# Performance work log

Hardware: AMD Instinct MI355X
Metric: run time of the kernel (lower is better)

The kernel has to match this reference:

```python
import jax, jax.numpy as jnp
import numpy as np

EPS = 1e-5

def rational(x, a, b):
    # Rational activation version 'A': P(x)/(1+|Q(x)|), deg(P)=5, deg(Q)=4 (no constant term)
    P = a[0] + x * (a[1] + x * (a[2] + x * (a[3] + x * (a[4] + x * a[5]))))
    Q = 1.0 + jnp.abs(x * (b[0] + x * (b[1] + x * (b[2] + x * b[3]))))
    return P / Q

def batch_norm(x, gamma, beta):
    # training-mode BN: per-channel batch statistics over (N,H,W), biased variance
    mean = jnp.mean(x, axis=(0, 2, 3), keepdims=True)
    var = jnp.var(x, axis=(0, 2, 3), keepdims=True)
    xn = (x - mean) * jax.lax.rsqrt(var + EPS)
    return xn * gamma[None, :, None, None] + beta[None, :, None, None]

def conv3x3(x, w):
    return jax.lax.conv_general_dilated(
        x, w, window_strides=(1, 1), padding='SAME',
        dimension_numbers=('NCHW', 'OIHW', 'NCHW'))

def multi_variant_rationals(out, ar, br, ag, bg, ab, bb):
    # channels 0::3 -> r rational, 1::3 -> g, 2::3 -> b; scatter back interleaved
    B, C, H, W = out.shape
    r = rational(out[:, 0::3], ar, br)  # (B, C//3, H, W)
    g = rational(out[:, 1::3], ag, bg)
    b = rational(out[:, 2::3], ab, bb)
    return jnp.stack([r, g, b], axis=2).reshape(B, C, H, W)

# Rational init coefficients (leaky-relu-like Pade approximant, standard rational_activations init)
_A0 = np.array([0.0218, 0.5, 1.5957, 1.1915, 0.5, 0.0891], dtype=np.float32)
_B0 = np.array([2.383, 0.0, 1.0, 0.0], dtype=np.float32)

def setup_inputs() -> dict:
    key = jax.random.key(0)
    ks = jax.random.split(key, 4)
    B, C, H, W = 64, 3, 512, 512
    x = jax.random.normal(ks[0], (B, C, H, W), dtype=jnp.float32)
    fan = C * 9
    w1 = jax.random.normal(ks[1], (C, C, 3, 3), dtype=jnp.float32) / np.sqrt(fan)
    w2 = jax.random.normal(ks[2], (C, C, 3, 3), dtype=jnp.float32) / np.sqrt(fan)
    g1 = jnp.ones((C,), jnp.float32); b1 = jnp.zeros((C,), jnp.float32)
    g2 = jnp.ones((C,), jnp.float32); b2 = jnp.zeros((C,), jnp.float32)
    ar = jnp.asarray(_A0); br = jnp.asarray(_B0)
    ag = jnp.asarray(_A0); bg = jnp.asarray(_B0)
    ab = jnp.asarray(_A0); bb = jnp.asarray(_B0)
    return {"x": x, "w1": w1, "g1": g1, "b1": b1, "ar": ar, "br": br,
            "ag": ag, "bg": bg, "ab": ab, "bb": bb, "w2": w2, "g2": g2, "b2": b2}

def reference(x, w1, g1, b1, ar, br, ag, bg, ab, bb, w2, g2, b2):
    out = conv3x3(x, w1)
    out = batch_norm(out, g1, b1)
    out = multi_variant_rationals(out, ar, br, ag, bg, ab, bb)
    out = conv3x3(out, w2)
    out = batch_norm(out, g2, b2)
    out = out + x  # identity shortcut (downsample=False)
    out = multi_variant_rationals(out, ar, br, ag, bg, ab, bb)
    return out
```

## Files before the change

### kernel.cpp

```cpp
#include <hip/hip_runtime.h>
#include <math.h>

#define HH 512
#define WW 512
#define NBATCH 64
#define PLANE (HH * WW)

#define TH2 16
#define NSTRIP (HH / TH2)
#define NWAVE (NBATCH * NSTRIP * 2)
#define NBLK2 (NWAVE / 4)
#define NPART NBLK2

#define TW 64
#define TH 16
#define NTILES (NBATCH * 8 * 32)
#define NTHR 256
#define XT_H (TH + 4)
#define XT_W (TW + 4)
#define ZT_H (TH + 2)
#define ZT_W (TW + 2)
#define X1_H (TH + 2)
#define X1_W (TW + 2)

#define Y1_ELEMS ((size_t)NBATCH * 3 * HH * WW)
#define WS_FAST_BYTES ((Y1_ELEMS + (size_t)NTILES * 6 + 16) * 4)

__device__ __forceinline__ float ratf(float v, const float* A, const float* B) {
  float p = fmaf(v, A[5], A[4]);
  p = fmaf(v, p, A[3]);
  p = fmaf(v, p, A[2]);
  p = fmaf(v, p, A[1]);
  p = fmaf(v, p, A[0]);
  float q = fmaf(v, B[3], B[2]);
  q = fmaf(v, q, B[1]);
  q = fmaf(v, q, B[0]);
  q *= v;
  float den = 1.0f + fabsf(q);
  return p * __builtin_amdgcn_rcpf(den);
}

__device__ __forceinline__ void block_reduce6_store(float s[6], float* __restrict__ dst) {
  __shared__ float red[4][6];
#pragma unroll
  for (int k = 0; k < 6; ++k) {
    float v = s[k];
#pragma unroll
    for (int off = 32; off; off >>= 1) v += __shfl_down(v, off, 64);
    s[k] = v;
  }
  int lane = threadIdx.x & 63, wv = threadIdx.x >> 6;
  if (lane == 0) {
#pragma unroll
    for (int k = 0; k < 6; ++k) red[wv][k] = s[k];
  }
  __syncthreads();
  if (threadIdx.x < 6) {
    dst[threadIdx.x] = red[0][threadIdx.x] + red[1][threadIdx.x] + red[2][threadIdx.x] + red[3][threadIdx.x];
  }
}

__global__ __launch_bounds__(256) void k_reduce(const float* __restrict__ partials, int n,
                                                const float* __restrict__ gamma,
                                                const float* __restrict__ beta,
                                                float* __restrict__ out6) {
  double s[6] = {0, 0, 0, 0, 0, 0};
  for (int j = threadIdx.x; j < n; j += 256) {
    const float* p = partials + (size_t)j * 6;
#pragma unroll
    for (int k = 0; k < 6; ++k) s[k] += (double)p[k];
  }
  __shared__ double red[256];
  __shared__ double tot[6];
  for (int k = 0; k < 6; ++k) {
    red[threadIdx.x] = s[k];
    __syncthreads();
    for (int off = 128; off; off >>= 1) {
      if (threadIdx.x < off) red[threadIdx.x] += red[threadIdx.x + off];
      __syncthreads();
    }
    if (threadIdx.x == 0) tot[k] = red[0];
    __syncthreads();
  }
  if (threadIdx.x < 3) {
    int c = threadIdx.x;
    double N = 16777216.0;
    double mean = tot[c] / N;
    double var = tot[3 + c] / N - mean * mean;
    double sc = (double)gamma[c] / sqrt(var + 1e-5);
    double sh = (double)beta[c] - mean * sc;
    out6[c] = (float)sc;
    out6[3 + c] = (float)sh;
  }
}


struct LRow {
  float4 v;
  float e;
  bool ok;
};
struct FRow {
  float4 v;
  float L, R;
};

__device__ __forceinline__ LRow load_row(const float* __restrict__ base, int gh, int c0,
                                         int lane, int elane, int eoff) {
  LRow r;
  r.v = make_float4(0.f, 0.f, 0.f, 0.f);
  r.e = 0.f;
  r.ok = ((unsigned)gh < (unsigned)HH);
  if (r.ok) {
    const float* p = base + (size_t)gh * WW + c0;
    r.v = *(const float4*)p;
    if (lane == elane) r.e = p[eoff];
  }
  return r;
}

__device__ __forceinline__ FRow fin1(const LRow& n, int lane, bool leftSeg) {
  FRow f;
  f.v = n.v;
  float Lp = __shfl_up(n.v.w, 1);
  float Rp = __shfl_down(n.v.x, 1);
  f.L = (lane == 0) ? (leftSeg ? 0.f : n.e) : Lp;
  f.R = (lane == 63) ? (leftSeg ? n.e : 0.f) : Rp;
  return f;
}

__device__ __forceinline__ FRow fin2(const LRow& n, int lane, bool leftSeg,
                                     float sc, float sh, const float* A, const float* B) {
  FRow f;
  if (!n.ok) {
    f.v = make_float4(0.f, 0.f, 0.f, 0.f);
    f.L = 0.f;
    f.R = 0.f;
    return f;
  }
  float4 z;
  z.x = ratf(fmaf(n.v.x, sc, sh), A, B);
  z.y = ratf(fmaf(n.v.y, sc, sh), A, B);
  z.z = ratf(fmaf(n.v.z, sc, sh), A, B);
  z.w = ratf(fmaf(n.v.w, sc, sh), A, B);
  float et = ratf(fmaf(n.e, sc, sh), A, B);
  float Lp = __shfl_up(z.w, 1);
  float Rp = __shfl_down(z.x, 1);
  f.v = z;
  f.L = (lane == 0) ? (leftSeg ? 0.f : et) : Lp;
  f.R = (lane == 63) ? (leftSeg ? et : 0.f) : Rp;
  return f;
}

__device__ __forceinline__ void conv_accum(const FRow (&F)[3][3], const float (&wr)[3][3][3][3],
                                           float4 (&acc)[3]) {
#pragma unroll
  for (int ci = 0; ci < 3; ++ci)
#pragma unroll
    for (int ky = 0; ky < 3; ++ky) {
      float s0 = F[ci][ky].L;
      float s1 = F[ci][ky].v.x;
      float s2 = F[ci][ky].v.y;
      float s3 = F[ci][ky].v.z;
      float s4 = F[ci][ky].v.w;
      float s5 = F[ci][ky].R;
#pragma unroll
      for (int co = 0; co < 3; ++co) {
        float w0 = wr[co][ci][ky][0], w1_ = wr[co][ci][ky][1], w2_ = wr[co][ci][ky][2];
        acc[co].x = fmaf(w0, s0, acc[co].x);
        acc[co].x = fmaf(w1_, s1, acc[co].x);
        acc[co].x = fmaf(w2_, s2, acc[co].x);
        acc[co].y = fmaf(w0, s1, acc[co].y);
        acc[co].y = fmaf(w1_, s2, acc[co].y);
        acc[co].y = fmaf(w2_, s3, acc[co].y);
        acc[co].z = fmaf(w0, s2, acc[co].z);
        acc[co].z = fmaf(w1_, s3, acc[co].z);
        acc[co].z = fmaf(w2_, s4, acc[co].z);
        acc[co].w = fmaf(w0, s3, acc[co].w);
        acc[co].w = fmaf(w1_, s4, acc[co].w);
        acc[co].w = fmaf(w2_, s5, acc[co].w);
      }
    }
}

__global__ __launch_bounds__(256) void k_conv1_v2(const float* __restrict__ x,
                                                  const float* __restrict__ w1,
                                                  float* __restrict__ y1,
                                                  float* __restrict__ partials) {
  int lane = threadIdx.x & 63;
  int wid = (blockIdx.x << 2) | (threadIdx.x >> 6);
  int seg = wid & 1;
  int strip = (wid >> 1) & (NSTRIP - 1);
  int b = wid >> 6;
  bool leftSeg = (seg == 0);
  int elane = leftSeg ? 63 : 0;
  int eoff = leftSeg ? 4 : -1;
  int c0 = (seg << 8) | (lane << 2);
  int h0 = strip * TH2;

  float wr[3][3][3][3];
#pragma unroll
  for (int o = 0; o < 3; ++o)
#pragma unroll
    for (int ci = 0; ci < 3; ++ci)
#pragma unroll
      for (int ky = 0; ky < 3; ++ky)
#pragma unroll
        for (int kx = 0; kx < 3; ++kx)
          wr[o][ci][ky][kx] = w1[((o * 3 + ci) * 3 + ky) * 3 + kx];

  const float* xb[3];
#pragma unroll
  for (int ci = 0; ci < 3; ++ci) xb[ci] = x + (size_t)(b * 3 + ci) * PLANE;
  float* yb = y1 + (size_t)(b * 3) * PLANE;

  FRow F[3][3];
  LRow N[3];
  {
    LRow P[3], Q[3];
#pragma unroll
    for (int ci = 0; ci < 3; ++ci) P[ci] = load_row(xb[ci], h0 - 1, c0, lane, elane, eoff);
#pragma unroll
    for (int ci = 0; ci < 3; ++ci) Q[ci] = load_row(xb[ci], h0, c0, lane, elane, eoff);
#pragma unroll
    for (int ci = 0; ci < 3; ++ci) N[ci] = load_row(xb[ci], h0 + 1, c0, lane, elane, eoff);
#pragma unroll
    for (int ci = 0; ci < 3; ++ci) {
      F[ci][0] = fin1(P[ci], lane, leftSeg);
      F[ci][1] = fin1(Q[ci], lane, leftSeg);
    }
  }

  float st[6] = {0.f, 0.f, 0.f, 0.f, 0.f, 0.f};
#pragma unroll 4
  for (int r = 0; r < TH2; ++r) {
#pragma unroll
    for (int ci = 0; ci < 3; ++ci) F[ci][2] = fin1(N[ci], lane, leftSeg);
    if (r < TH2 - 1) {
#pragma unroll
      for (int ci = 0; ci < 3; ++ci) N[ci] = load_row(xb[ci], h0 + r + 2, c0, lane, elane, eoff);
    }
    float4 acc[3];
    acc[0] = make_float4(0.f, 0.f, 0.f, 0.f);
    acc[1] = make_float4(0.f, 0.f, 0.f, 0.f);
    acc[2] = make_float4(0.f, 0.f, 0.f, 0.f);
    conv_accum(F, wr, acc);

    int gh = h0 + r;
    float* yrow = yb + (size_t)gh * WW + c0;
#pragma unroll
    for (int co = 0; co < 3; ++co) {
      *(float4*)(yrow + (size_t)co * PLANE) = acc[co];
      st[co] += (acc[co].x + acc[co].y) + (acc[co].z + acc[co].w);
      st[3 + co] += fmaf(acc[co].x, acc[co].x, acc[co].y * acc[co].y) +
                    fmaf(acc[co].z, acc[co].z, acc[co].w * acc[co].w);
    }
#pragma unroll
    for (int ci = 0; ci < 3; ++ci) {
      F[ci][0] = F[ci][1];
      F[ci][1] = F[ci][2];
    }
  }
  block_reduce6_store(st, partials + (size_t)blockIdx.x * 6);
}

__global__ __launch_bounds__(256) void k_conv2s_v2(const float* __restrict__ y1,
                                                   const float* __restrict__ w2,
                                                   const float* __restrict__ hdr,
                                                   const float* __restrict__ ar, const float* __restrict__ br,
                                                   const float* __restrict__ ag, const float* __restrict__ bg,
                                                   const float* __restrict__ ab_, const float* __restrict__ bb,
                                                   float* __restrict__ u,
                                                   float* __restrict__ partials) {
  int lane = threadIdx.x & 63;
  int wid = (blockIdx.x << 2) | (threadIdx.x >> 6);
  int seg = wid & 1;
  int strip = (wid >> 1) & (NSTRIP - 1);
  int b = wid >> 6;
  bool leftSeg = (seg == 0);
  int elane = leftSeg ? 63 : 0;
  int eoff = leftSeg ? 4 : -1;
  int c0 = (seg << 8) | (lane << 2);
  int h0 = strip * TH2;

  float sc1[3], sh1[3];
#pragma unroll
  for (int c = 0; c < 3; ++c) {
    sc1[c] = hdr[c];
    sh1[c] = hdr[3 + c];
  }
  float A[3][6], Bq[3][4];
#pragma unroll
  for (int i = 0; i < 6; ++i) { A[0][i] = ar[i]; A[1][i] = ag[i]; A[2][i] = ab_[i]; }
#pragma unroll
  for (int i = 0; i < 4; ++i) { Bq[0][i] = br[i]; Bq[1][i] = bg[i]; Bq[2][i] = bb[i]; }

  float wr[3][3][3][3];
#pragma unroll
  for (int o = 0; o < 3; ++o)
#pragma unroll
    for (int ci = 0; ci < 3; ++ci)
#pragma unroll
      for (int ky = 0; ky < 3; ++ky)
#pragma unroll
        for (int kx = 0; kx < 3; ++kx)
          wr[o][ci][ky][kx] = w2[((o * 3 + ci) * 3 + ky) * 3 + kx];

  const float* yb[3];
#pragma unroll
  for (int ci = 0; ci < 3; ++ci) yb[ci] = y1 + (size_t)(b * 3 + ci) * PLANE;
  float* ub = u + (size_t)(b * 3) * PLANE;

  FRow F[3][3];
  LRow N[3];
  {
    LRow P[3], Q[3];
#pragma unroll
    for (int ci = 0; ci < 3; ++ci) P[ci] = load_row(yb[ci], h0 - 1, c0, lane, elane, eoff);
#pragma unroll
    for (int ci = 0; ci < 3; ++ci) Q[ci] = load_row(yb[ci], h0, c0, lane, elane, eoff);
#pragma unroll
    for (int ci = 0; ci < 3; ++ci) N[ci] = load_row(yb[ci], h0 + 1, c0, lane, elane, eoff);
#pragma unroll
    for (int ci = 0; ci < 3; ++ci) {
      F[ci][0] = fin2(P[ci], lane, leftSeg, sc1[ci], sh1[ci], A[ci], Bq[ci]);
      F[ci][1] = fin2(Q[ci], lane, leftSeg, sc1[ci], sh1[ci], A[ci], Bq[ci]);
    }
  }

  float st[6] = {0.f, 0.f, 0.f, 0.f, 0.f, 0.f};
#pragma unroll 4
  for (int r = 0; r < TH2; ++r) {
#pragma unroll
    for (int ci = 0; ci < 3; ++ci)
      F[ci][2] = fin2(N[ci], lane, leftSeg, sc1[ci], sh1[ci], A[ci], Bq[ci]);
    if (r < TH2 - 1) {
#pragma unroll
      for (int ci = 0; ci < 3; ++ci) N[ci] = load_row(yb[ci], h0 + r + 2, c0, lane, elane, eoff);
    }
    float4 acc[3];
    acc[0] = make_float4(0.f, 0.f, 0.f, 0.f);
    acc[1] = make_float4(0.f, 0.f, 0.f, 0.f);
    acc[2] = make_float4(0.f, 0.f, 0.f, 0.f);
    conv_accum(F, wr, acc);

    int gh = h0 + r;
    float* urow = ub + (size_t)gh * WW + c0;
#pragma unroll
    for (int co = 0; co < 3; ++co) {
      *(float4*)(urow + (size_t)co * PLANE) = acc[co];
      st[co] += (acc[co].x + acc[co].y) + (acc[co].z + acc[co].w);
      st[3 + co] += fmaf(acc[co].x, acc[co].x, acc[co].y * acc[co].y) +
                    fmaf(acc[co].z, acc[co].z, acc[co].w * acc[co].w);
    }
#pragma unroll
    for (int ci = 0; ci < 3; ++ci) {
      F[ci][0] = F[ci][1];
      F[ci][1] = F[ci][2];
    }
  }
  block_reduce6_store(st, partials + (size_t)blockIdx.x * 6);
}

__global__ __launch_bounds__(256) void k_pointwise2(float* __restrict__ u,
                                                    const float* __restrict__ x,
                                                    const float* __restrict__ hdr,
                                                    const float* __restrict__ ar, const float* __restrict__ br,
                                                    const float* __restrict__ ag, const float* __restrict__ bg,
                                                    const float* __restrict__ ab_, const float* __restrict__ bb) {
  int plane = blockIdx.y;
  int c = plane % 3;
  const float* Ap = (c == 0) ? ar : ((c == 1) ? ag : ab_);
  const float* Bp = (c == 0) ? br : ((c == 1) ? bg : bb);
  float A[6], Bc[4];
#pragma unroll
  for (int i = 0; i < 6; ++i) A[i] = Ap[i];
#pragma unroll
  for (int i = 0; i < 4; ++i) Bc[i] = Bp[i];
  float sc2 = hdr[6 + c], sh2 = hdr[9 + c];

  size_t base = (size_t)plane * PLANE + (size_t)blockIdx.x * (256 * 8 * 4);
  const float4* xv = (const float4*)(x + base);
  float4* uv = (float4*)(u + base);
  float4 uu[8], xx[8];
#pragma unroll
  for (int k = 0; k < 8; ++k) uu[k] = uv[k * 256 + threadIdx.x];
#pragma unroll
  for (int k = 0; k < 8; ++k) xx[k] = xv[k * 256 + threadIdx.x];
#pragma unroll
  for (int k = 0; k < 8; ++k) {
    float4 o;
    o.x = ratf(fmaf(uu[k].x, sc2, sh2) + xx[k].x, A, Bc);
    o.y = ratf(fmaf(uu[k].y, sc2, sh2) + xx[k].y, A, Bc);
    o.z = ratf(fmaf(uu[k].z, sc2, sh2) + xx[k].z, A, Bc);
    o.w = ratf(fmaf(uu[k].w, sc2, sh2) + xx[k].w, A, Bc);
    uv[k * 256 + threadIdx.x] = o;
  }
}


__global__ __launch_bounds__(NTHR) void k_stats1(const float* __restrict__ x,
                                                 const float* __restrict__ w1,
                                                 float* __restrict__ partials) {
  __shared__ float xs[3][X1_H][X1_W];
  int bid = blockIdx.x;
  int tx = bid & 7, ty = (bid >> 3) & 31, b = bid >> 8;
  int h0 = ty * TH, w0 = tx * TW;

  const int NE = 3 * X1_H * X1_W;
  for (int i = threadIdx.x; i < NE; i += NTHR) {
    int c = i / (X1_H * X1_W);
    int rem = i - c * (X1_H * X1_W);
    int r = rem / X1_W, cc = rem - r * X1_W;
    int gh = h0 - 1 + r, gw = w0 - 1 + cc;
    float v = 0.f;
    if ((unsigned)gh < HH && (unsigned)gw < WW)
      v = x[(((size_t)b * 3 + c) * HH + gh) * WW + gw];
    xs[c][r][cc] = v;
  }
  float wr[3][3][3][3];
#pragma unroll
  for (int o = 0; o < 3; ++o)
#pragma unroll
    for (int ci = 0; ci < 3; ++ci)
#pragma unroll
      for (int ky = 0; ky < 3; ++ky)
#pragma unroll
        for (int kx = 0; kx < 3; ++kx)
          wr[o][ci][ky][kx] = w1[((o * 3 + ci) * 3 + ky) * 3 + kx];
  __syncthreads();

  int cc = threadIdx.x & 63;
  int rr0 = (threadIdx.x >> 6) * 4;
  float acc[4][3] = {};
#pragma unroll
  for (int ci = 0; ci < 3; ++ci)
#pragma unroll
    for (int kx = 0; kx < 3; ++kx) {
      float v[6];
#pragma unroll
      for (int i = 0; i < 6; ++i) v[i] = xs[ci][rr0 + i][cc + kx];
#pragma unroll
      for (int o = 0; o < 4; ++o)
#pragma unroll
        for (int ky = 0; ky < 3; ++ky) {
          float vv = v[o + ky];
#pragma unroll
          for (int co = 0; co < 3; ++co) acc[o][co] = fmaf(wr[co][ci][ky][kx], vv, acc[o][co]);
        }
    }
  float s[6] = {0.f, 0.f, 0.f, 0.f, 0.f, 0.f};
#pragma unroll
  for (int o = 0; o < 4; ++o)
#pragma unroll
    for (int co = 0; co < 3; ++co) {
      float y = acc[o][co];
      s[co] += y;
      s[3 + co] += y * y;
    }
  block_reduce6_store(s, partials + (size_t)bid * 6);
}

template <bool FINAL>
__global__ __launch_bounds__(NTHR) void k_fused(const float* __restrict__ x,
                                                const float* __restrict__ w1,
                                                const float* __restrict__ w2,
                                                const float* __restrict__ hdr,
                                                const float* __restrict__ ar, const float* __restrict__ br,
                                                const float* __restrict__ ag, const float* __restrict__ bg,
                                                const float* __restrict__ ab_, const float* __restrict__ bb,
                                                float* __restrict__ dst) {
  __shared__ float xs[3][XT_H][XT_W];
  __shared__ float zs[3][ZT_H][ZT_W];
  int bid = blockIdx.x;
  int tx = bid & 7, ty = (bid >> 3) & 31, b = bid >> 8;
  int h0 = ty * TH, w0 = tx * TW;

  const int NE = 3 * XT_H * XT_W;
  for (int i = threadIdx.x; i < NE; i += NTHR) {
    int c = i / (XT_H * XT_W);
    int rem = i - c * (XT_H * XT_W);
    int r = rem / XT_W, cc = rem - r * XT_W;
    int gh = h0 - 2 + r, gw = w0 - 2 + cc;
    float v = 0.f;
    if ((unsigned)gh < HH && (unsigned)gw < WW)
      v = x[(((size_t)b * 3 + c) * HH + gh) * WW + gw];
    xs[c][r][cc] = v;
  }

  float scale1[3], shift1[3];
#pragma unroll
  for (int c = 0; c < 3; ++c) {
    scale1[c] = hdr[c];
    shift1[c] = hdr[3 + c];
  }
  float A[3][6], Bq[3][4];
#pragma unroll
  for (int i = 0; i < 6; ++i) { A[0][i] = ar[i]; A[1][i] = ag[i]; A[2][i] = ab_[i]; }
#pragma unroll
  for (int i = 0; i < 4; ++i) { Bq[0][i] = br[i]; Bq[1][i] = bg[i]; Bq[2][i] = bb[i]; }

  float wr[3][3][3][3];
#pragma unroll
  for (int o = 0; o < 3; ++o)
#pragma unroll
    for (int ci = 0; ci < 3; ++ci)
#pragma unroll
      for (int ky = 0; ky < 3; ++ky)
#pragma unroll
        for (int kx = 0; kx < 3; ++kx)
          wr[o][ci][ky][kx] = w1[((o * 3 + ci) * 3 + ky) * 3 + kx];
  __syncthreads();

  for (int i = threadIdx.x; i < ZT_H * ZT_W; i += NTHR) {
    int r = i / ZT_W, cc = i - r * ZT_W;
    int gh = h0 - 1 + r, gw = w0 - 1 + cc;
    float z0 = 0.f, z1 = 0.f, z2 = 0.f;
    if ((unsigned)gh < HH && (unsigned)gw < WW) {
      float a0 = 0.f, a1 = 0.f, a2 = 0.f;
#pragma unroll
      for (int ci = 0; ci < 3; ++ci)
#pragma unroll
        for (int ky = 0; ky < 3; ++ky)
#pragma unroll
          for (int kx = 0; kx < 3; ++kx) {
            float v = xs[ci][r + ky][cc + kx];
            a0 = fmaf(wr[0][ci][ky][kx], v, a0);
            a1 = fmaf(wr[1][ci][ky][kx], v, a1);
            a2 = fmaf(wr[2][ci][ky][kx], v, a2);
          }
      z0 = ratf(fmaf(a0, scale1[0], shift1[0]), A[0], Bq[0]);
      z1 = ratf(fmaf(a1, scale1[1], shift1[1]), A[1], Bq[1]);
      z2 = ratf(fmaf(a2, scale1[2], shift1[2]), A[2], Bq[2]);
    }
    zs[0][r][cc] = z0;
    zs[1][r][cc] = z1;
    zs[2][r][cc] = z2;
  }

#pragma unroll
  for (int o = 0; o < 3; ++o)
#pragma unroll
    for (int ci = 0; ci < 3; ++ci)
#pragma unroll
      for (int ky = 0; ky < 3; ++ky)
#pragma unroll
        for (int kx = 0; kx < 3; ++kx)
          wr[o][ci][ky][kx] = w2[((o * 3 + ci) * 3 + ky) * 3 + kx];
  __syncthreads();

  int cc = threadIdx.x & 63;
  int rr0 = (threadIdx.x >> 6) * 4;
  float acc[4][3] = {};
#pragma unroll
  for (int ci = 0; ci < 3; ++ci)
#pragma unroll
    for (int kx = 0; kx < 3; ++kx) {
      float v[6];
#pragma unroll
      for (int i = 0; i < 6; ++i) v[i] = zs[ci][rr0 + i][cc + kx];
#pragma unroll
      for (int o = 0; o < 4; ++o)
#pragma unroll
        for (int ky = 0; ky < 3; ++ky) {
          float vv = v[o + ky];
#pragma unroll
          for (int co = 0; co < 3; ++co) acc[o][co] = fmaf(wr[co][ci][ky][kx], vv, acc[o][co]);
        }
    }

  if constexpr (FINAL) {
    float scale2[3], shift2[3];
#pragma unroll
    for (int c = 0; c < 3; ++c) {
      scale2[c] = hdr[6 + c];
      shift2[c] = hdr[9 + c];
    }
#pragma unroll
    for (int o = 0; o < 4; ++o) {
      int rr = rr0 + o;
#pragma unroll
      for (int co = 0; co < 3; ++co) {
        float y = fmaf(acc[o][co], scale2[co], shift2[co]);
        float v = y + xs[co][rr + 2][cc + 2];
        dst[(((size_t)b * 3 + co) * HH + (h0 + rr)) * WW + (w0 + cc)] = ratf(v, A[co], Bq[co]);
      }
    }
  } else {
    float s[6] = {0.f, 0.f, 0.f, 0.f, 0.f, 0.f};
#pragma unroll
    for (int o = 0; o < 4; ++o)
#pragma unroll
      for (int co = 0; co < 3; ++co) {
        float y = acc[o][co];
        s[co] += y;
        s[3 + co] += y * y;
      }
    block_reduce6_store(s, dst + (size_t)bid * 6);
  }
}

extern "C" void kernel_launch(void* const* d_in, const int* in_sizes, int n_in,
                              void* d_out, int out_size, void* d_ws, size_t ws_size,
                              hipStream_t stream) {
  const float* x  = (const float*)d_in[0];
  const float* w1 = (const float*)d_in[1];
  const float* g1 = (const float*)d_in[2];
  const float* b1 = (const float*)d_in[3];
  const float* ar = (const float*)d_in[4];
  const float* br = (const float*)d_in[5];
  const float* ag = (const float*)d_in[6];
  const float* bg = (const float*)d_in[7];
  const float* ab = (const float*)d_in[8];
  const float* bb = (const float*)d_in[9];
  const float* w2 = (const float*)d_in[10];
  const float* g2 = (const float*)d_in[11];
  const float* b2 = (const float*)d_in[12];
  float* out = (float*)d_out;

  if (ws_size >= WS_FAST_BYTES) {
    float* y1    = (float*)d_ws;
    float* part2 = (float*)d_ws + Y1_ELEMS;
    float* hdr   = part2 + (size_t)NPART * 6;
    float* part1 = out;

    k_conv1_v2<<<dim3(NBLK2), dim3(256), 0, stream>>>(x, w1, y1, part1);
    k_reduce<<<dim3(1), dim3(256), 0, stream>>>(part1, NPART, g1, b1, hdr);
    k_conv2s_v2<<<dim3(NBLK2), dim3(256), 0, stream>>>(y1, w2, hdr, ar, br, ag, bg, ab, bb, out, part2);
    k_reduce<<<dim3(1), dim3(256), 0, stream>>>(part2, NPART, g2, b2, hdr + 6);
    k_pointwise2<<<dim3(PLANE / (256 * 8 * 4), NBATCH * 3), dim3(256), 0, stream>>>(
        out, x, hdr, ar, br, ag, bg, ab, bb);
  } else {
    float* part1 = out;
    float* part2 = out + (size_t)NTILES * 6;
    float* hdr = (float*)d_ws;

    k_stats1<<<dim3(NTILES), dim3(NTHR), 0, stream>>>(x, w1, part1);
    k_reduce<<<dim3(1), dim3(256), 0, stream>>>(part1, NTILES, g1, b1, hdr);
    k_fused<false><<<dim3(NTILES), dim3(NTHR), 0, stream>>>(x, w1, w2, hdr, ar, br, ag, bg, ab, bb, part2);
    k_reduce<<<dim3(1), dim3(256), 0, stream>>>(part2, NTILES, g2, b2, hdr + 6);
    k_fused<true><<<dim3(NTILES), dim3(NTHR), 0, stream>>>(x, w1, w2, hdr, ar, br, ag, bg, ab, bb, out);
  }
}
```

Before: 621.5 us.

## Restructure conv row loop to scatter each input row into rotating accumulators

Both conv kernels now process each input row once, adding its contribution to three rotating output accumulators (one per kernel row) instead of keeping a three-row window of finished inputs and recomputing a full 3x3 stencil per output row. This drops the two extra FRow windows per channel in exchange for three float4 accumulator sets, with the aim of cutting register pressure and the row-shift copies. Output is emitted when an accumulator has received all three kernel rows. The main loop is hand-unrolled in groups of three with special prologue and epilogue steps, which adds some code size.

```diff
diff --git a/kernel.cpp b/kernel.cpp
--- a/kernel.cpp
+++ b/kernel.cpp
@@ -152,35 +152,75 @@
   return f;
 }
 
-__device__ __forceinline__ void conv_accum(const FRow (&F)[3][3], const float (&wr)[3][3][3][3],
-                                           float4 (&acc)[3]) {
+template <int KY>
+__device__ __forceinline__ void addrow(const FRow (&F)[3], const float (&wr)[3][3][3][3],
+                                       float4 (&acc)[3]) {
+#pragma unroll
+  for (int ci = 0; ci < 3; ++ci) {
+    float s0 = F[ci].L;
+    float s1 = F[ci].v.x;
+    float s2 = F[ci].v.y;
+    float s3 = F[ci].v.z;
+    float s4 = F[ci].v.w;
+    float s5 = F[ci].R;
+#pragma unroll
+    for (int co = 0; co < 3; ++co) {
+      float w0 = wr[co][ci][KY][0], w1_ = wr[co][ci][KY][1], w2_ = wr[co][ci][KY][2];
+      acc[co].x = fmaf(w0, s0, acc[co].x);
+      acc[co].x = fmaf(w1_, s1, acc[co].x);
+      acc[co].x = fmaf(w2_, s2, acc[co].x);
+      acc[co].y = fmaf(w0, s1, acc[co].y);
+      acc[co].y = fmaf(w1_, s2, acc[co].y);
+      acc[co].y = fmaf(w2_, s3, acc[co].y);
+      acc[co].z = fmaf(w0, s2, acc[co].z);
+      acc[co].z = fmaf(w1_, s3, acc[co].z);
+      acc[co].z = fmaf(w2_, s4, acc[co].z);
+      acc[co].w = fmaf(w0, s3, acc[co].w);
+      acc[co].w = fmaf(w1_, s4, acc[co].w);
+      acc[co].w = fmaf(w2_, s5, acc[co].w);
+    }
+  }
+}
+
+__device__ __forceinline__ void emit(float4 (&S)[3], float* __restrict__ dstb, int gh, int c0,
+                                     float (&st)[6], bool doStore) {
+  if (doStore) {
+    float* row = dstb + (size_t)gh * WW + c0;
+#pragma unroll
+    for (int co = 0; co < 3; ++co) {
+      float4 a = S[co];
+      *(float4*)(row + (size_t)co * PLANE) = a;
+      st[co] += (a.x + a.y) + (a.z + a.w);
+      st[3 + co] += fmaf(a.x, a.x, a.y * a.y) + fmaf(a.z, a.z, a.w * a.w);
+    }
+  }
+#pragma unroll
+  for (int co = 0; co < 3; ++co) S[co] = make_float4(0.f, 0.f, 0.f, 0.f);
+}
+
+__device__ __forceinline__ void adv1(FRow (&F)[3], LRow (&N)[3], const float* const (&xb)[3],
+                                     int gh_next, int c0, int lane, int elane, int eoff,
+                                     bool leftSeg, bool doLoad) {
+#pragma unroll
+  for (int ci = 0; ci < 3; ++ci) F[ci] = fin1(N[ci], lane, leftSeg);
+  if (doLoad) {
+#pragma unroll
+    for (int ci = 0; ci < 3; ++ci) N[ci] = load_row(xb[ci], gh_next, c0, lane, elane, eoff);
+  }
+}
+
+__device__ __forceinline__ void adv2(FRow (&F)[3], LRow (&N)[3], const float* const (&yb)[3],
+                                     int gh_next, int c0, int lane, int elane, int eoff,
+                                     bool leftSeg, bool doLoad,
+                                     const float (&sc1)[3], const float (&sh1)[3],
+                                     const float (&A)[3][6], const float (&Bq)[3][4]) {
 #pragma unroll
   for (int ci = 0; ci < 3; ++ci)
-#pragma unroll
-    for (int ky = 0; ky < 3; ++ky) {
-      float s0 = F[ci][ky].L;
-      float s1 = F[ci][ky].v.x;
-      float s2 = F[ci][ky].v.y;
-      float s3 = F[ci][ky].v.z;
-      float s4 = F[ci][ky].v.w;
-      float s5 = F[ci][ky].R;
-#pragma unroll
-      for (int co = 0; co < 3; ++co) {
-        float w0 = wr[co][ci][ky][0], w1_ = wr[co][ci][ky][1], w2_ = wr[co][ci][ky][2];
-        acc[co].x = fmaf(w0, s0, acc[co].x);
-        acc[co].x = fmaf(w1_, s1, acc[co].x);
-        acc[co].x = fmaf(w2_, s2, acc[co].x);
-        acc[co].y = fmaf(w0, s1, acc[co].y);
-        acc[co].y = fmaf(w1_, s2, acc[co].y);
-        acc[co].y = fmaf(w2_, s3, acc[co].y);
-        acc[co].z = fmaf(w0, s2, acc[co].z);
-        acc[co].z = fmaf(w1_, s3, acc[co].z);
-        acc[co].z = fmaf(w2_, s4, acc[co].z);
-        acc[co].w = fmaf(w0, s3, acc[co].w);
-        acc[co].w = fmaf(w1_, s4, acc[co].w);
-        acc[co].w = fmaf(w2_, s5, acc[co].w);
-      }
-    }
+    F[ci] = fin2(N[ci], lane, leftSeg, sc1[ci], sh1[ci], A[ci], Bq[ci]);
+  if (doLoad) {
+#pragma unroll
+    for (int ci = 0; ci < 3; ++ci) N[ci] = load_row(yb[ci], gh_next, c0, lane, elane, eoff);
+  }
 }
 
 __global__ __launch_bounds__(256) void k_conv1_v2(const float* __restrict__ x,
@@ -214,53 +254,48 @@
   for (int ci = 0; ci < 3; ++ci) xb[ci] = x + (size_t)(b * 3 + ci) * PLANE;
   float* yb = y1 + (size_t)(b * 3) * PLANE;
 
-  FRow F[3][3];
+  float4 s0[3], s1[3], s2[3];
+#pragma unroll
+  for (int co = 0; co < 3; ++co) {
+    s0[co] = make_float4(0.f, 0.f, 0.f, 0.f);
+    s1[co] = make_float4(0.f, 0.f, 0.f, 0.f);
+    s2[co] = make_float4(0.f, 0.f, 0.f, 0.f);
+  }
+  FRow F[3];
   LRow N[3];
   {
-    LRow P[3], Q[3];
-#pragma unroll
-    for (int ci = 0; ci < 3; ++ci) P[ci] = load_row(xb[ci], h0 - 1, c0, lane, elane, eoff);
-#pragma unroll
-    for (int ci = 0; ci < 3; ++ci) Q[ci] = load_row(xb[ci], h0, c0, lane, elane, eoff);
-#pragma unroll
-    for (int ci = 0; ci < 3; ++ci) N[ci] = load_row(xb[ci], h0 + 1, c0, lane, elane, eoff);
-#pragma unroll
-    for (int ci = 0; ci < 3; ++ci) {
-      F[ci][0] = fin1(P[ci], lane, leftSeg);
-      F[ci][1] = fin1(Q[ci], lane, leftSeg);
-    }
-  }
-
+    LRow C[3];
+#pragma unroll
+    for (int ci = 0; ci < 3; ++ci) C[ci] = load_row(xb[ci], h0 - 1, c0, lane, elane, eoff);
+#pragma unroll
+    for (int ci = 0; ci < 3; ++ci) N[ci] = load_row(xb[ci], h0, c0, lane, elane, eoff);
+#pragma unroll
+    for (int ci = 0; ci < 3; ++ci) F[ci] = fin1(C[ci], lane, leftSeg);
+  }
   float st[6] = {0.f, 0.f, 0.f, 0.f, 0.f, 0.f};
-#pragma unroll 4
-  for (int r = 0; r < TH2; ++r) {
-#pragma unroll
-    for (int ci = 0; ci < 3; ++ci) F[ci][2] = fin1(N[ci], lane, leftSeg);
-    if (r < TH2 - 1) {
-#pragma unroll
-      for (int ci = 0; ci < 3; ++ci) N[ci] = load_row(xb[ci], h0 + r + 2, c0, lane, elane, eoff);
-    }
-    float4 acc[3];
-    acc[0] = make_float4(0.f, 0.f, 0.f, 0.f);
-    acc[1] = make_float4(0.f, 0.f, 0.f, 0.f);
-    acc[2] = make_float4(0.f, 0.f, 0.f, 0.f);
-    conv_accum(F, wr, acc);
-
-    int gh = h0 + r;
-    float* yrow = yb + (size_t)gh * WW + c0;
-#pragma unroll
-    for (int co = 0; co < 3; ++co) {
-      *(float4*)(yrow + (size_t)co * PLANE) = acc[co];
-      st[co] += (acc[co].x + acc[co].y) + (acc[co].z + acc[co].w);
-      st[3 + co] += fmaf(acc[co].x, acc[co].x, acc[co].y * acc[co].y) +
-                    fmaf(acc[co].z, acc[co].z, acc[co].w * acc[co].w);
-    }
-#pragma unroll
-    for (int ci = 0; ci < 3; ++ci) {
-      F[ci][0] = F[ci][1];
-      F[ci][1] = F[ci][2];
-    }
-  }
+
+#define C1STEP(SA, SB, SC, T, DOSTORE, DOLOAD, DOADV)                                   \
+  do {                                                                                  \
+    addrow<0>(F, wr, SA);                                                               \
+    addrow<1>(F, wr, SB);                                                               \
+    addrow<2>(F, wr, SC);                                                               \
+    emit(SC, yb, h0 + (T)-2, c0, st, (DOSTORE));                                        \
+    if (DOADV) adv1(F, N, xb, h0 + (T) + 1, c0, lane, elane, eoff, leftSeg, (DOLOAD));  \
+  } while (0)
+
+  C1STEP(s0, s2, s1, 0, false, true, true);
+  C1STEP(s1, s0, s2, 1, false, true, true);
+  C1STEP(s2, s1, s0, 2, true, true, true);
+  for (int tb = 3; tb <= 12; tb += 3) {
+    C1STEP(s0, s2, s1, tb, true, true, true);
+    C1STEP(s1, s0, s2, tb + 1, true, true, true);
+    C1STEP(s2, s1, s0, tb + 2, true, true, true);
+  }
+  C1STEP(s0, s2, s1, 15, true, true, true);
+  C1STEP(s1, s0, s2, 16, true, false, true);
+  C1STEP(s2, s1, s0, 17, true, false, false);
+#undef C1STEP
+
   block_reduce6_store(st, partials + (size_t)blockIdx.x * 6);
 }
 
@@ -311,54 +346,50 @@
   for (int ci = 0; ci < 3; ++ci) yb[ci] = y1 + (size_t)(b * 3 + ci) * PLANE;
   float* ub = u + (size_t)(b * 3) * PLANE;
 
-  FRow F[3][3];
+  float4 s0[3], s1[3], s2[3];
+#pragma unroll
+  for (int co = 0; co < 3; ++co) {
+    s0[co] = make_float4(0.f, 0.f, 0.f, 0.f);
+    s1[co] = make_float4(0.f, 0.f, 0.f, 0.f);
+    s2[co] = make_float4(0.f, 0.f, 0.f, 0.f);
+  }
+  FRow F[3];
   LRow N[3];
   {
-    LRow P[3], Q[3];
-#pragma unroll
-    for (int ci = 0; ci < 3; ++ci) P[ci] = load_row(yb[ci], h0 - 1, c0, lane, elane, eoff);
-#pragma unroll
-    for (int ci = 0; ci < 3; ++ci) Q[ci] = load_row(yb[ci], h0, c0, lane, elane, eoff);
-#pragma unroll
-    for (int ci = 0; ci < 3; ++ci) N[ci] = load_row(yb[ci], h0 + 1, c0, lane, elane, eoff);
-#pragma unroll
-    for (int ci = 0; ci < 3; ++ci) {
-      F[ci][0] = fin2(P[ci], lane, leftSeg, sc1[ci], sh1[ci], A[ci], Bq[ci]);
-      F[ci][1] = fin2(Q[ci], lane, leftSeg, sc1[ci], sh1[ci], A[ci], Bq[ci]);
-    }
-  }
-
+    LRow C[3];
+#pragma unroll
+    for (int ci = 0; ci < 3; ++ci) C[ci] = load_row(yb[ci], h0 - 1, c0, lane, elane, eoff);
+#pragma unroll
+    for (int ci = 0; ci < 3; ++ci) N[ci] = load_row(yb[ci], h0, c0, lane, elane, eoff);
+#pragma unroll
+    for (int ci = 0; ci < 3; ++ci)
+      F[ci] = fin2(C[ci], lane, leftSeg, sc1[ci], sh1[ci], A[ci], Bq[ci]);
+  }
   float st[6] = {0.f, 0.f, 0.f, 0.f, 0.f, 0.f};
-#pragma unroll 4
-  for (int r = 0; r < TH2; ++r) {
-#pragma unroll
-    for (int ci = 0; ci < 3; ++ci)
-      F[ci][2] = fin2(N[ci], lane, leftSeg, sc1[ci], sh1[ci], A[ci], Bq[ci]);
-    if (r < TH2 - 1) {
-#pragma unroll
-      for (int ci = 0; ci < 3; ++ci) N[ci] = load_row(yb[ci], h0 + r + 2, c0, lane, elane, eoff);
-    }
-    float4 acc[3];
-    acc[0] = make_float4(0.f, 0.f, 0.f, 0.f);
-    acc[1] = make_float4(0.f, 0.f, 0.f, 0.f);
-    acc[2] = make_float4(0.f, 0.f, 0.f, 0.f);
-    conv_accum(F, wr, acc);
-
-    int gh = h0 + r;
-    float* urow = ub + (size_t)gh * WW + c0;
-#pragma unroll
-    for (int co = 0; co < 3; ++co) {
-      *(float4*)(urow + (size_t)co * PLANE) = acc[co];
-      st[co] += (acc[co].x + acc[co].y) + (acc[co].z + acc[co].w);
-      st[3 + co] += fmaf(acc[co].x, acc[co].x, acc[co].y * acc[co].y) +
-                    fmaf(acc[co].z, acc[co].z, acc[co].w * acc[co].w);
-    }
-#pragma unroll
-    for (int ci = 0; ci < 3; ++ci) {
-      F[ci][0] = F[ci][1];
-      F[ci][1] = F[ci][2];
-    }
-  }
+
+#define C2STEP(SA, SB, SC, T, DOSTORE, DOLOAD, DOADV)                                   \
+  do {                                                                                  \
+    addrow<0>(F, wr, SA);                                                               \
+    addrow<1>(F, wr, SB);                                                               \
+    addrow<2>(F, wr, SC);                                                               \
+    emit(SC, ub, h0 + (T)-2, c0, st, (DOSTORE));                                        \
+    if (DOADV)                                                                          \
+      adv2(F, N, yb, h0 + (T) + 1, c0, lane, elane, eoff, leftSeg, (DOLOAD), sc1, sh1, A, Bq); \
+  } while (0)
+
+  C2STEP(s0, s2, s1, 0, false, true, true);
+  C2STEP(s1, s0, s2, 1, false, true, true);
+  C2STEP(s2, s1, s0, 2, true, true, true);
+  for (int tb = 3; tb <= 12; tb += 3) {
+    C2STEP(s0, s2, s1, tb, true, true, true);
+    C2STEP(s1, s0, s2, tb + 1, true, true, true);
+    C2STEP(s2, s1, s0, tb + 2, true, true, true);
+  }
+  C2STEP(s0, s2, s1, 15, true, true, true);
+  C2STEP(s1, s0, s2, 16, true, false, true);
+  C2STEP(s2, s1, s0, 17, true, false, false);
+#undef C2STEP
+
   block_reduce6_store(st, partials + (size_t)blockIdx.x * 6);
 }
 
```

Result: slower. 662.1 us (+6.5%).
